# Performance work log

Measured on AMD Instinct MI355X. Metric: run time of the kernel, lower is better.

Reference implementation:

```python
import jax, jax.numpy as jnp
import numpy as np

B = 65536          # batch rows
FULL = 1024        # full_dim
E = 64             # number of block experts
W = FULL // E      # block width = 16 (equal contiguous slices)
HID = 64           # expert hidden
GH = 32            # gate hidden
SCALE = 0.05


def setup_inputs() -> dict:
    key = jax.random.key(0)
    ks = jax.random.split(key, 12)
    n = jax.random.normal
    return {
        "x": n(ks[0], (B, FULL), dtype=jnp.float32),
        # gate: Linear(FULL,32) -> ReLU -> Linear(32,E)
        "gw1": n(ks[1], (FULL, GH), dtype=jnp.float32) * SCALE,
        "gb1": n(ks[2], (GH,), dtype=jnp.float32) * SCALE,
        "gw2": n(ks[3], (GH, E), dtype=jnp.float32) * SCALE,
        "gb2": n(ks[4], (E,), dtype=jnp.float32) * SCALE,
        # stacked per-expert MLP params: W->HID->HID//2->1
        "ew1": n(ks[5], (E, W, HID), dtype=jnp.float32) * SCALE,
        "eb1": n(ks[6], (E, HID), dtype=jnp.float32) * SCALE,
        "ew2": n(ks[7], (E, HID, HID // 2), dtype=jnp.float32) * SCALE,
        "eb2": n(ks[8], (E, HID // 2), dtype=jnp.float32) * SCALE,
        "ew3": n(ks[9], (E, HID // 2, 1), dtype=jnp.float32) * SCALE,
        "eb3": n(ks[10], (E, 1), dtype=jnp.float32) * SCALE,
    }


def reference(x, gw1, gb1, gw2, gb2, ew1, eb1, ew2, eb2, ew3, eb3):
    # gate -> soft weights over experts, [B, E]
    g = jax.nn.relu(x @ gw1 + gb1)
    w = jax.nn.softmax(g @ gw2 + gb2, axis=1)
    # equal contiguous blocks: x[:, e*W:(e+1)*W] == x.reshape(B, E, W)[:, e]
    xb = x.reshape(x.shape[0], E, W)
    h = jax.nn.relu(jnp.einsum("bew,ewh->beh", xb, ew1) + eb1)      # [B,E,HID]
    h = jax.nn.relu(jnp.einsum("beh,eho->beo", h, ew2) + eb2)       # [B,E,HID//2]
    logits = (jnp.einsum("beh,eho->beo", h, ew3) + eb3)[..., 0]     # [B,E]
    return jnp.sum(w * logits, axis=1, keepdims=True)               # [B,1]
```

## Files before the change

kernel.cpp:

```cpp
#include <hip/hip_runtime.h>

typedef __attribute__((ext_vector_type(8))) short short8;
typedef __attribute__((ext_vector_type(4))) short short4_;
typedef __attribute__((ext_vector_type(4))) float float4_;

#define NGROUP 16
#define EPG 4
#define GBLK_US 14336
#define OFF_A2_US 4096
#define OFF_AG_US 12288
#define OFF_TAIL_US 229376
#define N_A1 65536
#define N_A2 131072
#define N_AG 32768
#define N_TOT 231424

#define ROWS_PB 128
#define STASH_LD 130

__device__ __forceinline__ unsigned short f2bf(float f) {
  unsigned u = __builtin_bit_cast(unsigned, f);
  u += 0x7FFFu + ((u >> 16) & 1u);
  return (unsigned short)(u >> 16);
}
__device__ __forceinline__ float bf2f(unsigned short s) {
  unsigned u = ((unsigned)s) << 16;
  return __builtin_bit_cast(float, u);
}
__device__ __forceinline__ float4_ MFMA(short8 a, short8 b, float4_ c) {
  return __builtin_amdgcn_mfma_f32_16x16x32_bf16(a, b, c, 0, 0, 0);
}
__device__ __forceinline__ float4_ relu4(float4_ v) {
  v[0] = fmaxf(v[0], 0.f); v[1] = fmaxf(v[1], 0.f);
  v[2] = fmaxf(v[2], 0.f); v[3] = fmaxf(v[3], 0.f);
  return v;
}
__device__ __forceinline__ short8 swap32(short8 v) {
  union { short8 s; int i[4]; } u; u.s = v;
#pragma unroll
  for (int k = 0; k < 4; ++k) u.i[k] = __shfl_xor(u.i[k], 32);
  return u.s;
}

__global__ void moe_setup(const float* __restrict__ gw1,
                          const float* __restrict__ gw2,
                          const float* __restrict__ ew1,
                          const float* __restrict__ ew2,
                          unsigned short* __restrict__ wsp)
{
  for (int i = blockIdx.x * blockDim.x + threadIdx.x; i < N_TOT;
       i += gridDim.x * blockDim.x) {
    if (i < N_A1) {
      int g = i >> 12, a = i & 4095;
      int j = a & 7, l = (a >> 3) & 31, mt = (a >> 8) & 3, e = (a >> 10) & 3;
      int k = ((l >> 4) << 3) + j;
      int h = 16 * mt + (l & 15);
      int E = g * 4 + e;
      wsp[g * GBLK_US + a] = f2bf(ew1[(E * 16 + k) * 64 + h]);
    } else if (i < N_A1 + N_A2) {
      int i2 = i - N_A1;
      int g = i2 >> 13, b = i2 & 8191;
      int j = b & 3, l = (b >> 2) & 63, c = (b >> 8) & 3, mt2 = (b >> 10) & 1, e = (b >> 11) & 3;
      int q = l >> 4;
      int h1 = 16 * c + 4 * q + j;
      int h2 = 16 * mt2 + (l & 15);
      int E = g * 4 + e;
      wsp[g * GBLK_US + OFF_A2_US + b] = f2bf(ew2[(E * 64 + h1) * 32 + h2]);
    } else if (i < N_A1 + N_A2 + N_AG) {
      int i3 = i - (N_A1 + N_A2);
      int g = i3 >> 11, a = i3 & 2047;
      int j = a & 7, l = (a >> 3) & 63, kc = (a >> 9) & 1, mt = (a >> 10) & 1;
      int q = l >> 4;
      int col = g * 64 + kc * 32 + q * 8 + j;
      int gh = 16 * mt + (l & 15);
      wsp[g * GBLK_US + OFF_AG_US + a] = f2bf(gw1[col * 32 + gh]);
    } else {
      int d = i - (N_A1 + N_A2 + N_AG);
      int j = d & 3, l = (d >> 2) & 63, c = (d >> 8) & 1, mt3 = (d >> 9) & 3;
      int q = l >> 4;
      int gh = 16 * c + 4 * q + j;
      int e = 16 * mt3 + (l & 15);
      wsp[OFF_TAIL_US + d] = f2bf(gw2[gh * 64 + e]);
    }
  }
}

__global__ __launch_bounds__(512, 4) void moe_main(
    const float* __restrict__ x,
    const float* __restrict__ gb1,
    const float* __restrict__ gb2,
    const float* __restrict__ eb1,
    const float* __restrict__ eb2,
    const float* __restrict__ ew3,
    const float* __restrict__ eb3,
    const unsigned short* __restrict__ wsp,
    float* __restrict__ out)
{
  __shared__ __align__(16) unsigned short sStage[GBLK_US];
  __shared__ unsigned short sStash[64 * STASH_LD];

  const int tid = threadIdx.x;
  const int wave = tid >> 6;
  const int lane = tid & 63;
  const int q = lane >> 4;
  const int n = lane & 15;
  const int wrow = wave * 16;
  const size_t rowBase0 = (size_t)blockIdx.x * ROWS_PB + wrow;

  const short8 zero8 = {0, 0, 0, 0, 0, 0, 0, 0};

  float4_ cg[2];
  cg[0] = (float4_){0.f, 0.f, 0.f, 0.f};
  cg[1] = (float4_){0.f, 0.f, 0.f, 0.f};

  for (int g = 0; g < NGROUP; ++g) {
    __syncthreads();
    {
      const uint4* src = (const uint4*)(wsp + (size_t)g * GBLK_US);
      uint4* dst = (uint4*)sStage;
#pragma unroll
      for (int it = 0; it < 4; ++it) {
        int idx = tid + it * 512;
        if (idx < 1792) dst[idx] = src[idx];
      }
    }
    __syncthreads();

    short8 bx[2];
#pragma unroll
    for (int kc = 0; kc < 2; ++kc) {
      const float* px = x + (rowBase0 + n) * 1024 + g * 64 + kc * 32 + q * 8;
      float4_ f0 = *(const float4_*)px;
      float4_ f1 = *(const float4_*)(px + 4);
      short8 v;
      v[0] = f2bf(f0[0]); v[1] = f2bf(f0[1]); v[2] = f2bf(f0[2]); v[3] = f2bf(f0[3]);
      v[4] = f2bf(f1[0]); v[5] = f2bf(f1[1]); v[6] = f2bf(f1[2]); v[7] = f2bf(f1[3]);
      bx[kc] = v;
    }

#pragma unroll
    for (int m = 0; m < 2; ++m)
#pragma unroll
      for (int kc = 0; kc < 2; ++kc) {
        short8 a = *(const short8*)(sStage + OFF_AG_US + ((m * 2 + kc) * 64 + lane) * 8);
        cg[m] = MFMA(a, bx[kc], cg[m]);
      }

    for (int e = 0; e < EPG; ++e) {
      const int E = g * EPG + e;
      short8 b1 = bx[e >> 1];
      if (e & 1) b1 = swap32(b1);
      b1 = (lane < 32) ? b1 : zero8;

      float4_ c1[4];
#pragma unroll
      for (int m = 0; m < 4; ++m)
        c1[m] = *(const float4_*)(eb1 + E * 64 + 16 * m + 4 * q);
#pragma unroll
      for (int m = 0; m < 4; ++m) {
        short8 a1 = zero8;
        if (lane < 32) a1 = *(const short8*)(sStage + ((e * 4 + m) * 32 + lane) * 8);
        c1[m] = MFMA(a1, b1, c1[m]);
      }
#pragma unroll
      for (int m = 0; m < 4; ++m) c1[m] = relu4(c1[m]);

      float4_ c2[2];
#pragma unroll
      for (int m = 0; m < 2; ++m)
        c2[m] = *(const float4_*)(eb2 + E * 32 + 16 * m + 4 * q);
#pragma unroll
      for (int c = 0; c < 4; ++c) {
        short8 b2 = zero8;
        b2[0] = f2bf(c1[c][0]); b2[1] = f2bf(c1[c][1]);
        b2[2] = f2bf(c1[c][2]); b2[3] = f2bf(c1[c][3]);
#pragma unroll
        for (int m = 0; m < 2; ++m) {
          short4_ lo = *(const short4_*)(sStage + OFF_A2_US + (((e * 2 + m) * 4 + c) * 64 + lane) * 4);
          short8 a2 = {lo[0], lo[1], lo[2], lo[3], 0, 0, 0, 0};
          c2[m] = MFMA(a2, b2, c2[m]);
        }
      }
      float p = 0.f;
#pragma unroll
      for (int m = 0; m < 2; ++m) {
        float4_ cc = relu4(c2[m]);
        float4_ w3v = *(const float4_*)(ew3 + E * 32 + 16 * m + 4 * q);
        p += cc[0] * w3v[0] + cc[1] * w3v[1] + cc[2] * w3v[2] + cc[3] * w3v[3];
      }
      p += __shfl_xor(p, 16);
      p += __shfl_xor(p, 32);
      p += eb3[E];
      if (lane < 16) sStash[E * STASH_LD + wrow + lane] = f2bf(p);
    }
  }

  short8 bg[2];
#pragma unroll
  for (int c = 0; c < 2; ++c) {
    float4_ gv = *(const float4_*)(gb1 + 16 * c + 4 * q);
    float4_ v = cg[c];
    v[0] = fmaxf(v[0] + gv[0], 0.f); v[1] = fmaxf(v[1] + gv[1], 0.f);
    v[2] = fmaxf(v[2] + gv[2], 0.f); v[3] = fmaxf(v[3] + gv[3], 0.f);
    short8 pv = zero8;
    pv[0] = f2bf(v[0]); pv[1] = f2bf(v[1]); pv[2] = f2bf(v[2]); pv[3] = f2bf(v[3]);
    bg[c] = pv;
  }
  float4_ c3[4];
#pragma unroll
  for (int m = 0; m < 4; ++m)
    c3[m] = *(const float4_*)(gb2 + 16 * m + 4 * q);
#pragma unroll
  for (int m = 0; m < 4; ++m)
#pragma unroll
    for (int c = 0; c < 2; ++c) {
      short4_ lo = *(const short4_*)(wsp + OFF_TAIL_US + ((m * 2 + c) * 64 + lane) * 4);
      short8 a = {lo[0], lo[1], lo[2], lo[3], 0, 0, 0, 0};
      c3[m] = MFMA(a, bg[c], c3[m]);
    }
  float mx = -1e30f;
#pragma unroll
  for (int m = 0; m < 4; ++m) {
    mx = fmaxf(mx, c3[m][0]); mx = fmaxf(mx, c3[m][1]);
    mx = fmaxf(mx, c3[m][2]); mx = fmaxf(mx, c3[m][3]);
  }
  mx = fmaxf(mx, __shfl_xor(mx, 16));
  mx = fmaxf(mx, __shfl_xor(mx, 32));
  float s = 0.f, o = 0.f;
#pragma unroll
  for (int m = 0; m < 4; ++m)
#pragma unroll
    for (int i = 0; i < 4; ++i) {
      int e = 16 * m + 4 * q + i;
      float w = __expf(c3[m][i] - mx);
      s += w;
      o += w * bf2f(sStash[e * STASH_LD + wrow + n]);
    }
  s += __shfl_xor(s, 16);
  s += __shfl_xor(s, 32);
  o += __shfl_xor(o, 16);
  o += __shfl_xor(o, 32);
  if (lane < 16) out[rowBase0 + lane] = o / s;
}

extern "C" void kernel_launch(void* const* d_in, const int* in_sizes, int n_in,
                              void* d_out, int out_size, void* d_ws, size_t ws_size,
                              hipStream_t stream) {
  const float* x   = (const float*)d_in[0];
  const float* gw1 = (const float*)d_in[1];
  const float* gb1 = (const float*)d_in[2];
  const float* gw2 = (const float*)d_in[3];
  const float* gb2 = (const float*)d_in[4];
  const float* ew1 = (const float*)d_in[5];
  const float* eb1 = (const float*)d_in[6];
  const float* ew2 = (const float*)d_in[7];
  const float* eb2 = (const float*)d_in[8];
  const float* ew3 = (const float*)d_in[9];
  const float* eb3 = (const float*)d_in[10];
  unsigned short* wsp = (unsigned short*)d_ws;
  float* out = (float*)d_out;

  moe_setup<<<256, 256, 0, stream>>>(gw1, gw2, ew1, ew2, wsp);
  moe_main<<<512, 512, 0, stream>>>(x, gb1, gb2, eb1, eb2, ew3, eb3, wsp, out);
}
```

Before: 462.2 us.

## Double-buffer weight staging and prefetch next x slice into registers

Makes the per-group weight stage in shared memory double-buffered. The next group's weights and x slice are loaded into registers while the current group is computed, then stored to the alternate buffer with one barrier per group. This is meant to hide global-load latency and drop one barrier per iteration. In exchange, shared memory per block roughly doubles and register use grows, which may lower occupancy. The setup kernel grid is also doubled.

```diff
diff --git a/kernel.cpp b/kernel.cpp
--- a/kernel.cpp
+++ b/kernel.cpp
@@ -96,7 +96,7 @@
     const unsigned short* __restrict__ wsp,
     float* __restrict__ out)
 {
-  __shared__ __align__(16) unsigned short sStage[GBLK_US];
+  __shared__ __align__(16) unsigned short sStage[2][GBLK_US];
   __shared__ unsigned short sStash[64 * STASH_LD];
 
   const int tid = threadIdx.x;
@@ -113,25 +113,52 @@
   cg[0] = (float4_){0.f, 0.f, 0.f, 0.f};
   cg[1] = (float4_){0.f, 0.f, 0.f, 0.f};
 
+  uint4 stg[4];
+  {
+    const uint4* src = (const uint4*)wsp;
+#pragma unroll
+    for (int it = 0; it < 4; ++it) {
+      int idx = tid + it * 512;
+      if (idx < 1792) stg[it] = src[idx];
+    }
+  }
+  float4_ xf[4];
+  {
+    const float* px = x + (rowBase0 + n) * 1024 + q * 8;
+    xf[0] = *(const float4_*)px;        xf[1] = *(const float4_*)(px + 4);
+    xf[2] = *(const float4_*)(px + 32); xf[3] = *(const float4_*)(px + 36);
+  }
+  {
+    uint4* dst = (uint4*)sStage[0];
+#pragma unroll
+    for (int it = 0; it < 4; ++it) {
+      int idx = tid + it * 512;
+      if (idx < 1792) dst[idx] = stg[it];
+    }
+  }
+  __syncthreads();
+
   for (int g = 0; g < NGROUP; ++g) {
-    __syncthreads();
-    {
-      const uint4* src = (const uint4*)(wsp + (size_t)g * GBLK_US);
-      uint4* dst = (uint4*)sStage;
+    const unsigned short* sCur = sStage[g & 1];
+    const bool more = (g + 1 < NGROUP);
+
+    float4_ xn[4];
+    if (more) {
+      const uint4* src = (const uint4*)(wsp + (size_t)(g + 1) * GBLK_US);
 #pragma unroll
       for (int it = 0; it < 4; ++it) {
         int idx = tid + it * 512;
-        if (idx < 1792) dst[idx] = src[idx];
-      }
-    }
-    __syncthreads();
+        if (idx < 1792) stg[it] = src[idx];
+      }
+      const float* px = x + (rowBase0 + n) * 1024 + (g + 1) * 64 + q * 8;
+      xn[0] = *(const float4_*)px;        xn[1] = *(const float4_*)(px + 4);
+      xn[2] = *(const float4_*)(px + 32); xn[3] = *(const float4_*)(px + 36);
+    }
 
     short8 bx[2];
 #pragma unroll
     for (int kc = 0; kc < 2; ++kc) {
-      const float* px = x + (rowBase0 + n) * 1024 + g * 64 + kc * 32 + q * 8;
-      float4_ f0 = *(const float4_*)px;
-      float4_ f1 = *(const float4_*)(px + 4);
+      float4_ f0 = xf[kc * 2], f1 = xf[kc * 2 + 1];
       short8 v;
       v[0] = f2bf(f0[0]); v[1] = f2bf(f0[1]); v[2] = f2bf(f0[2]); v[3] = f2bf(f0[3]);
       v[4] = f2bf(f1[0]); v[5] = f2bf(f1[1]); v[6] = f2bf(f1[2]); v[7] = f2bf(f1[3]);
@@ -142,7 +169,7 @@
     for (int m = 0; m < 2; ++m)
 #pragma unroll
       for (int kc = 0; kc < 2; ++kc) {
-        short8 a = *(const short8*)(sStage + OFF_AG_US + ((m * 2 + kc) * 64 + lane) * 8);
+        short8 a = *(const short8*)(sCur + OFF_AG_US + ((m * 2 + kc) * 64 + lane) * 8);
         cg[m] = MFMA(a, bx[kc], cg[m]);
       }
 
@@ -159,7 +186,7 @@
 #pragma unroll
       for (int m = 0; m < 4; ++m) {
         short8 a1 = zero8;
-        if (lane < 32) a1 = *(const short8*)(sStage + ((e * 4 + m) * 32 + lane) * 8);
+        if (lane < 32) a1 = *(const short8*)(sCur + ((e * 4 + m) * 32 + lane) * 8);
         c1[m] = MFMA(a1, b1, c1[m]);
       }
 #pragma unroll
@@ -176,7 +203,7 @@
         b2[2] = f2bf(c1[c][2]); b2[3] = f2bf(c1[c][3]);
 #pragma unroll
         for (int m = 0; m < 2; ++m) {
-          short4_ lo = *(const short4_*)(sStage + OFF_A2_US + (((e * 2 + m) * 4 + c) * 64 + lane) * 4);
+          short4_ lo = *(const short4_*)(sCur + OFF_A2_US + (((e * 2 + m) * 4 + c) * 64 + lane) * 4);
           short8 a2 = {lo[0], lo[1], lo[2], lo[3], 0, 0, 0, 0};
           c2[m] = MFMA(a2, b2, c2[m]);
         }
@@ -192,6 +219,18 @@
       p += __shfl_xor(p, 32);
       p += eb3[E];
       if (lane < 16) sStash[E * STASH_LD + wrow + lane] = f2bf(p);
+    }
+
+    if (more) {
+      uint4* dst = (uint4*)sStage[(g & 1) ^ 1];
+#pragma unroll
+      for (int it = 0; it < 4; ++it) {
+        int idx = tid + it * 512;
+        if (idx < 1792) dst[idx] = stg[it];
+      }
+      __syncthreads();
+#pragma unroll
+      for (int i = 0; i < 4; ++i) xf[i] = xn[i];
     }
   }
 
@@ -260,6 +299,6 @@
   unsigned short* wsp = (unsigned short*)d_ws;
   float* out = (float*)d_out;
 
-  moe_setup<<<256, 256, 0, stream>>>(gw1, gw2, ew1, ew2, wsp);
+  moe_setup<<<512, 256, 0, stream>>>(gw1, gw2, ew1, ew2, wsp);
   moe_main<<<512, 512, 0, stream>>>(x, gb1, gb2, eb1, eb2, ew3, eb3, wsp, out);
 }
```

After: 514.8 us. 11.4% more time.
